# Kernel optimization log

Hardware: AMD Instinct MI355X
Metric: run time of the kernel (lower is better)

## Reference

```python
import jax, jax.numpy as jnp
import numpy as np

T = 0.07  # temperature from init default


def _l2norm(x):
    return x / jnp.linalg.norm(x, axis=1, keepdims=True)


def setup_inputs() -> dict:
    key = jax.random.key(0)
    ks = jax.random.split(key, 12)
    B, D, K = 512, 128, 4096
    G = M = 131072
    return {
        "feat": jax.random.normal(ks[0], (B, D), jnp.float32),
        "label": jax.random.randint(ks[1], (B,), 0, 2),
        "out": jnp.zeros((B, K + 1), jnp.float32),   # unused by forward
        "name": jnp.arange(B),                        # unused by forward
        "y": jax.random.randint(ks[2], (B,), 0, G),   # unused by forward
        "memory_feat_gbm": jax.random.normal(ks[3], (G, D), jnp.float32),
        "memory_prob_gbm": jax.random.uniform(ks[4], (G,), jnp.float32),
        "memory_feat_mate": jax.random.normal(ks[5], (M, D), jnp.float32),
        "memory_prob_mate": jax.random.uniform(ks[6], (M,), jnp.float32),
        "idx_n_g": jax.random.randint(ks[7], (K, 1), 0, G),
        "idx_p_g": jax.random.randint(ks[8], (1, 1), 0, G // 4),
        "idx_n_m": jax.random.randint(ks[9], (K, 1), 0, M),
        "idx_p_m": jax.random.randint(ks[10], (1, 1), 0, M // 4),
    }


def reference(feat, label, out, name, y, memory_feat_gbm, memory_prob_gbm,
              memory_feat_mate, memory_prob_mate, idx_n_g, idx_p_g, idx_n_m, idx_p_m):
    # __init__ normalizes the memory banks once
    mfg = _l2norm(memory_feat_gbm)
    mfm = _l2norm(memory_feat_mate)
    feat_n = _l2norm(feat)  # [B, D]
    output_size = mfg.shape[0]

    # gather positive / negative prototypes (all rows unit-norm, so
    # cosine_similarity == dot product)
    wp_g = mfg[idx_p_g.ravel()]   # [1, D]
    wn_g = mfg[idx_n_g.ravel()]   # [K, D]
    wp_m = mfm[idx_p_m.ravel()]   # [1, D]
    wn_m = mfm[idx_n_m.ravel()]   # [K, D]

    # label==0 (gbm): pos from gbm bank, negs from mate bank; label==1 mirrored
    row_gbm = jnp.concatenate([feat_n @ wp_g.T, feat_n @ wn_m.T], axis=1)   # [B, K+1]
    row_mate = jnp.concatenate([feat_n @ wp_m.T, feat_n @ wn_g.T], axis=1)  # [B, K+1]
    sims = jnp.where((label == 0)[:, None], row_gbm, row_mate)

    # use_softmax=False path: exp(s/T) / Z with Z set from first batch (treated as constant)
    e = jnp.exp(sims / T)
    Z = jax.lax.stop_gradient(e.mean() * output_size)
    out_feature_p_n = e / Z

    # confident cluster members + current batch (data-dependent sizes; eager jax)
    mask_g = memory_prob_gbm > 0.5
    mask_m = memory_prob_mate > 0.6
    feature_clu_all = jnp.concatenate([mfg[mask_g], mfm[mask_m], feat_n], axis=0)
    gt_clu_all = jnp.concatenate([
        jnp.zeros((int(mask_g.sum()),), label.dtype),
        jnp.ones((int(mask_m.sum()),), label.dtype),
        label,
    ], axis=0)
    return out_feature_p_n, feature_clu_all, gt_clu_all
```

## Files before the change

kernel.cpp:

```cpp
#include <hip/hip_runtime.h>
#include <math.h>


#define TINV 14.2857142857142857f
#define JT 64
#define BT2 64

typedef __attribute__((ext_vector_type(8))) short bfrag;
typedef __attribute__((ext_vector_type(4))) float ffrag;

__device__ __forceinline__ float wredsum64(float v) {
#pragma unroll
  for (int m = 32; m > 0; m >>= 1) v += __shfl_xor(v, m, 64);
  return v;
}

__device__ __forceinline__ unsigned short f2bf(float x) {
  unsigned u = __float_as_uint(x);
  u += 0x7fffu + ((u >> 16) & 1u);
  return (unsigned short)(u >> 16);
}

__device__ __forceinline__ bfrag ldsread(const short* base, int row, int kb) {
  return *(const bfrag*)((const char*)base + row * 256 +
                         (kb ^ ((row & 7) << 4)));
}
__device__ __forceinline__ void ldswrite(short* base, int row, int kb,
                                         bfrag v) {
  *(bfrag*)((char*)base + row * 256 + (kb ^ ((row & 7) << 4))) = v;
}

__global__ __launch_bounds__(256) void k_stageA(
    const float* __restrict__ feat, const int* __restrict__ label,
    const float* __restrict__ mfg, const float* __restrict__ pg,
    const float* __restrict__ mfm, const float* __restrict__ pm,
    const int* __restrict__ idxpg, const int* __restrict__ idxpm,
    float* __restrict__ outp, long long cluTail, long long gtTail,
    int* __restrict__ bucket, int* __restrict__ n0p,
    int* __restrict__ cg, int* __restrict__ cm,
    float* __restrict__ posPartials,
    int B, int K1, int G, int M,
    int nCountBlk, int nFeatBlk, int nPosBlk) {
  int bid = blockIdx.x, t = threadIdx.x;

  if (bid < nCountBlk) {
    __shared__ int s[8];
    int i = bid * 256 + t;
    int a = (i < G) && (pg[i] > 0.5f);
    int b = (i < M) && (pm[i] > 0.6f);
    unsigned long long ba = __ballot(a), bb = __ballot(b);
    int lane = t & 63, w = t >> 6;
    if (lane == 0) { s[w] = __popcll(ba); s[4 + w] = __popcll(bb); }
    __syncthreads();
    if (t == 0) cg[bid] = s[0] + s[1] + s[2] + s[3];
    if (t == 1) cm[bid] = s[4] + s[5] + s[6] + s[7];
    return;
  }
  bid -= nCountBlk;

  if (bid < nFeatBlk) {
    int gid = bid * 256 + t;
    int w = gid >> 6, lane = gid & 63;
    if (w < B) {
      float2 v = ((const float2*)feat)[(long long)w * 64 + lane];
      float sq = wredsum64(v.x * v.x + v.y * v.y);
      float inv = rsqrtf(sq);
      ((float2*)(outp + cluTail))[(long long)w * 64 + lane] =
          make_float2(v.x * inv, v.y * inv);
      if (lane == 0) outp[gtTail + w] = (float)label[w];
    }
    return;
  }
  bid -= nFeatBlk;

  if (bid < nPosBlk) {
    __shared__ float ps[4];
    int gid = bid * 256 + t;
    int w = gid >> 6, lane = gid & 63, lw = t >> 6;
    float e = 0.f;
    if (w < B) {
      int lab = label[w];
      const float* bank = lab ? mfm : mfg;
      long long row = lab ? idxpm[0] : idxpg[0];
      float2 wv = ((const float2*)(bank + row * 128))[lane];
      float2 fv = ((const float2*)feat)[(long long)w * 64 + lane];
      float dot = wredsum64(fv.x * wv.x + fv.y * wv.y);
      float sqw = wredsum64(wv.x * wv.x + wv.y * wv.y);
      float sqf = wredsum64(fv.x * fv.x + fv.y * fv.y);
      e = expf(dot * rsqrtf(sqw) * rsqrtf(sqf) * TINV);
      if (lane == 0) outp[(long long)w * K1] = e;
    }
    if (lane == 0) ps[lw] = e;
    __syncthreads();
    if (t == 0) posPartials[bid] = ps[0] + ps[1] + ps[2] + ps[3];
    return;
  }

  {
    __shared__ int sc[512];
    int t2 = t + 256;
    int m0 = (t < B) ? (label[t] == 0 ? 1 : 0) : 0;
    int m1 = (t2 < B) ? (label[t2] == 0 ? 1 : 0) : 0;
    sc[t] = m0; sc[t2] = m1;
    __syncthreads();
    for (int off = 1; off < 512; off <<= 1) {
      int u0 = (t >= off) ? sc[t - off] : 0;
      int u1 = (t2 >= off) ? sc[t2 - off] : 0;
      __syncthreads();
      sc[t] += u0; sc[t2] += u1;
      __syncthreads();
    }
    int n0 = (B > 0) ? sc[B - 1] : 0;
    if (t < B) {
      int incl = sc[t];
      if (m0) bucket[incl - 1] = t; else bucket[n0 + t - incl] = t;
    }
    if (t2 < B) {
      int incl = sc[t2];
      if (m1) bucket[incl - 1] = t2; else bucket[n0 + t2 - incl] = t2;
    }
    if (t == 0) *n0p = n0;
  }
}

__global__ __launch_bounds__(256) void k_stageB(
    const float* __restrict__ featn, const int* __restrict__ bucket,
    const int* __restrict__ n0ptr,
    const float* __restrict__ mfg, const float* __restrict__ mfm,
    const int* __restrict__ idxng, const int* __restrict__ idxnm,
    float* __restrict__ out0, float* __restrict__ partials,
    int B, int K, int K1, int simsGx) {
  __shared__ __align__(16) short wlds[64 * 128];
  __shared__ __align__(16) short flds[64 * 128];
  __shared__ float invw[64];
  __shared__ float bs[4];
  int t = threadIdx.x;
  int pidx = (int)blockIdx.x;
  int bx = pidx % simsGx, by = pidx / simsGx;
  int n0 = *n0ptr;
  int nb0 = (n0 + BT2 - 1) / BT2;
  int lab, p0, cnt;
  if (by < nb0) {
    lab = 0; p0 = by * BT2; cnt = min(BT2, n0 - p0);
  } else {
    int k = by - nb0; p0 = n0 + k * BT2;
    int n1 = B - n0; cnt = min(BT2, n1 - k * BT2); lab = 1;
  }
  if (cnt <= 0) { if (t == 0) partials[pidx] = 0.f; return; }
  const float* bank = lab == 0 ? mfm : mfg;
  const int* idxN   = lab == 0 ? idxnm : idxng;
  int j0 = bx * JT;

#pragma unroll
  for (int q = 0; q < 4; q++) {
    int slot = q * 256 + t;
    int row = slot >> 4, ch = slot & 15;
    long long srow = idxN[j0 + row];
    const float4* gp = (const float4*)(bank + srow * 128 + ch * 8);
    float4 x0 = gp[0], x1 = gp[1];
    bfrag h;
    h[0] = (short)f2bf(x0.x); h[1] = (short)f2bf(x0.y);
    h[2] = (short)f2bf(x0.z); h[3] = (short)f2bf(x0.w);
    h[4] = (short)f2bf(x1.x); h[5] = (short)f2bf(x1.y);
    h[6] = (short)f2bf(x1.z); h[7] = (short)f2bf(x1.w);
    ldswrite(wlds, row, ch * 16, h);
    float s = x0.x*x0.x + x0.y*x0.y + x0.z*x0.z + x0.w*x0.w +
              x1.x*x1.x + x1.y*x1.y + x1.z*x1.z + x1.w*x1.w;
    s += __shfl_xor(s, 1, 64);
    s += __shfl_xor(s, 2, 64);
    s += __shfl_xor(s, 4, 64);
    s += __shfl_xor(s, 8, 64);
    if (ch == 0) invw[row] = rsqrtf(s);
  }
#pragma unroll
  for (int q = 0; q < 4; q++) {
    int slot = q * 256 + t;
    int row = slot >> 4, ch = slot & 15;
    bfrag h;
#pragma unroll
    for (int i = 0; i < 8; i++) h[i] = 0;
    if (row < cnt) {
      int bg = bucket[p0 + row];
      const float4* gp = (const float4*)(featn + (long long)bg * 128 + ch * 8);
      float4 x0 = gp[0], x1 = gp[1];
      h[0] = (short)f2bf(x0.x); h[1] = (short)f2bf(x0.y);
      h[2] = (short)f2bf(x0.z); h[3] = (short)f2bf(x0.w);
      h[4] = (short)f2bf(x1.x); h[5] = (short)f2bf(x1.y);
      h[6] = (short)f2bf(x1.z); h[7] = (short)f2bf(x1.w);
    }
    ldswrite(flds, row, ch * 16, h);
  }
  __syncthreads();

  int l = t & 63, wv = t >> 6;
  int wj = wv & 1, wb = wv >> 1;
  int colb = l & 15, kg = l >> 4;
  ffrag acc00 = {0.f, 0.f, 0.f, 0.f};
  ffrag acc01 = {0.f, 0.f, 0.f, 0.f};
  ffrag acc10 = {0.f, 0.f, 0.f, 0.f};
  ffrag acc11 = {0.f, 0.f, 0.f, 0.f};
#pragma unroll
  for (int ks = 0; ks < 4; ks++) {
    int kb = ks * 64 + kg * 16;
    bfrag a0 = ldsread(flds, wb * 32 + colb,      kb);
    bfrag a1 = ldsread(flds, wb * 32 + 16 + colb, kb);
    bfrag b0 = ldsread(wlds, wj * 32 + colb,      kb);
    bfrag b1 = ldsread(wlds, wj * 32 + 16 + colb, kb);
    acc00 = __builtin_amdgcn_mfma_f32_16x16x32_bf16(a0, b0, acc00, 0, 0, 0);
    acc01 = __builtin_amdgcn_mfma_f32_16x16x32_bf16(a0, b1, acc01, 0, 0, 0);
    acc10 = __builtin_amdgcn_mfma_f32_16x16x32_bf16(a1, b0, acc10, 0, 0, 0);
    acc11 = __builtin_amdgcn_mfma_f32_16x16x32_bf16(a1, b1, acc11, 0, 0, 0);
  }

  float mysum = 0.f;
  int rowg = l >> 4;
  auto epi = [&](const ffrag& A, int bt, int jt) {
    int bl = wb * 32 + bt * 16 + rowg * 4;
    int jl = wj * 32 + jt * 16 + colb;
    float iw = invw[jl];
#pragma unroll
    for (int r = 0; r < 4; r++) {
      int b2 = bl + r;
      if (b2 < cnt) {
        int bg = bucket[p0 + b2];
        float e = expf(A[r] * iw * TINV);
        out0[(long long)bg * K1 + 1 + j0 + jl] = e;
        mysum += e;
      }
    }
  };
  epi(acc00, 0, 0); epi(acc01, 0, 1); epi(acc10, 1, 0); epi(acc11, 1, 1);

  float wsum = wredsum64(mysum);
  if ((t & 63) == 0) bs[t >> 6] = wsum;
  __syncthreads();
  if (t == 0) partials[pidx] = bs[0] + bs[1] + bs[2] + bs[3];
}

__global__ __launch_bounds__(256) void k_stageD(
    const float* __restrict__ mfg, const float* __restrict__ mfm,
    const float* __restrict__ pg, const float* __restrict__ pm,
    const int* __restrict__ cg, const int* __restrict__ cm,
    float* __restrict__ outp, long long cluBase, long long gtBase,
    int G, int M, int NB, int nGatherBlk,
    float* __restrict__ out0, const float* __restrict__ partials, int nPart,
    double factor, long long n4) {
  int t = threadIdx.x;

  if ((int)blockIdx.x < nGatherBlk) {
    __shared__ int red[4];
    __shared__ int woff[4];
    __shared__ int selRow[256];
    int bid = blockIdx.x;
    int bankId = bid / NB;
    int cb = bid - bankId * NB;
    const float* probs = bankId ? pm : pg;
    const float* rows  = bankId ? mfm : mfg;
    float thr = bankId ? 0.6f : 0.5f;
    int Nelem = bankId ? M : G;
    int lane = t & 63, w = t >> 6;

    int j0 = t, j1 = t + 256;
    int s = 0;
    if (bankId == 0) {
      if (j0 < cb) s += cg[j0];
      if (j1 < cb && j1 < NB) s += cg[j1];
    } else {
      if (j0 < NB) s += cg[j0];
      if (j1 < NB) s += cg[j1];
      if (j0 < cb) s += cm[j0];
      if (j1 < cb && j1 < NB) s += cm[j1];
    }
#pragma unroll
    for (int m = 32; m > 0; m >>= 1) s += __shfl_xor(s, m, 64);
    if (lane == 0) red[w] = s;

    int i = cb * 256 + t;
    int f = (i < Nelem) && (probs[i] > thr);
    unsigned long long mb = __ballot(f);
    if (lane == 0) woff[w] = __popcll(mb);
    __syncthreads();

    long long off = (long long)red[0] + red[1] + red[2] + red[3];
    int pre = 0;
#pragma unroll
    for (int q = 0; q < 3; q++)
      if (q < w) pre += woff[q];
    int S = woff[0] + woff[1] + woff[2] + woff[3];
    unsigned long long below = lane ? ((~0ull) >> (64 - lane)) : 0ull;
    if (f) selRow[pre + __popcll(mb & below)] = i;
    __syncthreads();
    if (S == 0) return;

    float labv = (float)bankId;
    int hw = t >> 5, l = t & 31;
    for (int r0 = hw * 4; r0 < S; r0 += 32) {
      int r1 = r0 + 1, r2 = r0 + 2, r3 = r0 + 3;
      int s0 = selRow[r0];
      int s1 = selRow[r1 < S ? r1 : r0];
      int s2 = selRow[r2 < S ? r2 : r0];
      int s3 = selRow[r3 < S ? r3 : r0];
      float4 v0 = ((const float4*)(rows + (long long)s0 * 128))[l];
      float4 v1 = ((const float4*)(rows + (long long)s1 * 128))[l];
      float4 v2 = ((const float4*)(rows + (long long)s2 * 128))[l];
      float4 v3 = ((const float4*)(rows + (long long)s3 * 128))[l];
      float q0 = v0.x*v0.x + v0.y*v0.y + v0.z*v0.z + v0.w*v0.w;
      float q1 = v1.x*v1.x + v1.y*v1.y + v1.z*v1.z + v1.w*v1.w;
      float q2 = v2.x*v2.x + v2.y*v2.y + v2.z*v2.z + v2.w*v2.w;
      float q3 = v3.x*v3.x + v3.y*v3.y + v3.z*v3.z + v3.w*v3.w;
#pragma unroll
      for (int m = 16; m > 0; m >>= 1) {
        q0 += __shfl_xor(q0, m, 64);
        q1 += __shfl_xor(q1, m, 64);
        q2 += __shfl_xor(q2, m, 64);
        q3 += __shfl_xor(q3, m, 64);
      }
      float i0 = rsqrtf(q0), i1 = rsqrtf(q1), i2 = rsqrtf(q2), i3 = rsqrtf(q3);
      long long d0 = off + r0;
      ((float4*)(outp + cluBase + d0 * 128))[l] =
          make_float4(v0.x*i0, v0.y*i0, v0.z*i0, v0.w*i0);
      if (l == 0) outp[gtBase + d0] = labv;
      if (r1 < S) {
        long long d = off + r1;
        ((float4*)(outp + cluBase + d * 128))[l] =
            make_float4(v1.x*i1, v1.y*i1, v1.z*i1, v1.w*i1);
        if (l == 0) outp[gtBase + d] = labv;
      }
      if (r2 < S) {
        long long d = off + r2;
        ((float4*)(outp + cluBase + d * 128))[l] =
            make_float4(v2.x*i2, v2.y*i2, v2.z*i2, v2.w*i2);
        if (l == 0) outp[gtBase + d] = labv;
      }
      if (r3 < S) {
        long long d = off + r3;
        ((float4*)(outp + cluBase + d * 128))[l] =
            make_float4(v3.x*i3, v3.y*i3, v3.z*i3, v3.w*i3);
        if (l == 0) outp[gtBase + d] = labv;
      }
    }
    return;
  }

  __shared__ double sd[256];
  double s = 0.0;
  for (int i = t; i < nPart; i += 256) s += (double)partials[i];
  sd[t] = s;
  __syncthreads();
  for (int off = 128; off > 0; off >>= 1) {
    if (t < off) sd[t] += sd[t + off];
    __syncthreads();
  }
  float sc = (float)(factor / sd[0]);
  long long base = (long long)((int)blockIdx.x - nGatherBlk) * 256 + t;
  long long stride = (long long)(gridDim.x - nGatherBlk) * 256;
  for (long long i = base; i < n4; i += stride) {
    float4 v = ((float4*)out0)[i];
    v.x *= sc; v.y *= sc; v.z *= sc; v.w *= sc;
    ((float4*)out0)[i] = v;
  }
}

extern "C" void kernel_launch(void* const* d_in, const int* in_sizes, int n_in,
                              void* d_out, int out_size, void* d_ws,
                              size_t ws_size, hipStream_t stream) {
  const float* feat  = (const float*)d_in[0];
  const int*   label = (const int*)d_in[1];
  const float* mfg   = (const float*)d_in[5];
  const float* pg    = (const float*)d_in[6];
  const float* mfm   = (const float*)d_in[7];
  const float* pm    = (const float*)d_in[8];
  const int*   idxng = (const int*)d_in[9];
  const int*   idxpg = (const int*)d_in[10];
  const int*   idxnm = (const int*)d_in[11];
  const int*   idxpm = (const int*)d_in[12];
  float* outp = (float*)d_out;

  const int B = in_sizes[1];
  const int D = 128;
  const int K = in_sizes[9];
  const int G = in_sizes[6];
  const int M = in_sizes[8];
  const int K1 = K + 1;

  const long long C0 = (long long)B * K1;
  const long long R = ((long long)out_size - C0) / (D + 1);
  const long long G0 = C0 + R * D;
  const long long cluTail = C0 + (R - B) * (long long)D;
  const long long gtTail = G0 + (R - B);

  const float* featn = outp + cluTail;

  char* wsb = (char*)d_ws;
  size_t o = 0;
  auto alloc = [&](size_t bytes) -> char* {
    char* p = wsb + o;
    o = (o + bytes + 255) & ~(size_t)255;
    return p;
  };
  const int simsGx = K / JT;
  const int simsGy = B / BT2 + 2;
  const int nPartSims = simsGx * simsGy;
  const int nPosBlk = (B * 64 + 255) / 256;
  float* partials = (float*)alloc(sizeof(float) * (nPartSims + nPosBlk));
  int* bucket = (int*)alloc(sizeof(int) * B);
  int* n0p = (int*)alloc(sizeof(int) * 4);
  const int NB = ((G > M ? G : M) + 255) / 256;
  int* cg = (int*)alloc(sizeof(int) * NB);
  int* cm = (int*)alloc(sizeof(int) * NB);
  (void)ws_size; (void)n_in;

  const int nFeatBlk = (B * 64 + 255) / 256;
  const int gridA = NB + nFeatBlk + nPosBlk + 1;
  const int gridB = nPartSims;
  const int nGatherBlk = 2 * NB;
  const int nScaleBlk = 1024;
  const int gridD = nGatherBlk + nScaleBlk;

  k_stageA<<<gridA, 256, 0, stream>>>(
      feat, label, mfg, pg, mfm, pm, idxpg, idxpm,
      outp, cluTail, gtTail, bucket, n0p, cg, cm,
      partials + nPartSims, B, K1, G, M, NB, nFeatBlk, nPosBlk);

  k_stageB<<<gridB, 256, 0, stream>>>(
      featn, bucket, n0p, mfg, mfm, idxng, idxnm,
      outp, partials, B, K, K1, simsGx);

  double factor = (double)B * (double)K1 / (double)G;
  k_stageD<<<gridD, 256, 0, stream>>>(
      mfg, mfm, pg, pm, cg, cm, outp, C0, G0, G, M, NB, nGatherBlk,
      outp, partials, nPartSims + nPosBlk, factor, C0 / 4);
}
```

Before: 44.76 us.

## Shrink gather chunks to 64 rows, stage rows in LDS, use nontemporal stores

Stage A now writes per-wavefront (64-element) popcounts instead of per-block counts. Stage D then launches one gather block per 64-element chunk instead of per 256, which quadruples the gather grid and spreads the compaction across more blocks. Each block stages selected rows in LDS, computes norms from per-lane partial sums there, and writes normalized rows with nontemporal stores. The prefix-offset loop now reads four times as many counts per block, and the extra LDS staging adds syncs and shared-memory traffic per block.

```diff
diff --git a/kernel.cpp b/kernel.cpp
--- a/kernel.cpp
+++ b/kernel.cpp
@@ -8,8 +8,15 @@
 
 typedef __attribute__((ext_vector_type(8))) short bfrag;
 typedef __attribute__((ext_vector_type(4))) float ffrag;
+typedef __attribute__((ext_vector_type(4))) float f4v;
 
 __device__ __forceinline__ float wredsum64(float v) {
+#pragma unroll
+  for (int m = 32; m > 0; m >>= 1) v += __shfl_xor(v, m, 64);
+  return v;
+}
+
+__device__ __forceinline__ int wredsum64i(int v) {
 #pragma unroll
   for (int m = 32; m > 0; m >>= 1) v += __shfl_xor(v, m, 64);
   return v;
@@ -37,23 +44,22 @@
     const int* __restrict__ idxpg, const int* __restrict__ idxpm,
     float* __restrict__ outp, long long cluTail, long long gtTail,
     int* __restrict__ bucket, int* __restrict__ n0p,
-    int* __restrict__ cg, int* __restrict__ cm,
+    int* __restrict__ cg64, int* __restrict__ cm64,
     float* __restrict__ posPartials,
     int B, int K1, int G, int M,
     int nCountBlk, int nFeatBlk, int nPosBlk) {
   int bid = blockIdx.x, t = threadIdx.x;
 
   if (bid < nCountBlk) {
-    __shared__ int s[8];
     int i = bid * 256 + t;
     int a = (i < G) && (pg[i] > 0.5f);
     int b = (i < M) && (pm[i] > 0.6f);
     unsigned long long ba = __ballot(a), bb = __ballot(b);
     int lane = t & 63, w = t >> 6;
-    if (lane == 0) { s[w] = __popcll(ba); s[4 + w] = __popcll(bb); }
-    __syncthreads();
-    if (t == 0) cg[bid] = s[0] + s[1] + s[2] + s[3];
-    if (t == 1) cm[bid] = s[4] + s[5] + s[6] + s[7];
+    if (lane == 0) {
+      cg64[bid * 4 + w] = __popcll(ba);
+      cm64[bid * 4 + w] = __popcll(bb);
+    }
     return;
   }
   bid -= nCountBlk;
@@ -240,103 +246,98 @@
 __global__ __launch_bounds__(256) void k_stageD(
     const float* __restrict__ mfg, const float* __restrict__ mfm,
     const float* __restrict__ pg, const float* __restrict__ pm,
-    const int* __restrict__ cg, const int* __restrict__ cm,
+    const int* __restrict__ cg64, const int* __restrict__ cm64,
     float* __restrict__ outp, long long cluBase, long long gtBase,
-    int G, int M, int NB, int nGatherBlk,
+    int G, int M, int NG64, int nGatherBlk,
     float* __restrict__ out0, const float* __restrict__ partials, int nPart,
     double factor, long long n4) {
   int t = threadIdx.x;
 
   if ((int)blockIdx.x < nGatherBlk) {
+    __shared__ float rowbuf[64][132];
+    __shared__ float psum[64][33];
+    __shared__ float invw[64];
+    __shared__ int selRow[64];
     __shared__ int red[4];
-    __shared__ int woff[4];
-    __shared__ int selRow[256];
+    __shared__ int Ssh;
     int bid = blockIdx.x;
-    int bankId = bid / NB;
-    int cb = bid - bankId * NB;
+    int bankId = bid / NG64;
+    int g = bid - bankId * NG64;
     const float* probs = bankId ? pm : pg;
     const float* rows  = bankId ? mfm : mfg;
     float thr = bankId ? 0.6f : 0.5f;
     int Nelem = bankId ? M : G;
     int lane = t & 63, w = t >> 6;
 
-    int j0 = t, j1 = t + 256;
     int s = 0;
-    if (bankId == 0) {
-      if (j0 < cb) s += cg[j0];
-      if (j1 < cb && j1 < NB) s += cg[j1];
-    } else {
-      if (j0 < NB) s += cg[j0];
-      if (j1 < NB) s += cg[j1];
-      if (j0 < cb) s += cm[j0];
-      if (j1 < cb && j1 < NB) s += cm[j1];
-    }
-#pragma unroll
-    for (int m = 32; m > 0; m >>= 1) s += __shfl_xor(s, m, 64);
+    for (int j = t; j < NG64; j += 256) {
+      if (bankId == 0) {
+        if (j < g) s += cg64[j];
+      } else {
+        s += cg64[j];
+        if (j < g) s += cm64[j];
+      }
+    }
+    s = wredsum64i(s);
     if (lane == 0) red[w] = s;
 
-    int i = cb * 256 + t;
-    int f = (i < Nelem) && (probs[i] > thr);
-    unsigned long long mb = __ballot(f);
-    if (lane == 0) woff[w] = __popcll(mb);
-    __syncthreads();
-
+    if (t < 64) {
+      int c = g * 64 + t;
+      int f = (c < Nelem) && (probs[c] > thr);
+      unsigned long long mb = __ballot(f);
+      unsigned long long below = t ? ((~0ull) >> (64 - t)) : 0ull;
+      if (f) selRow[__popcll(mb & below)] = c;
+      if (t == 0) Ssh = (int)__popcll(mb);
+    }
+    __syncthreads();
+    int S = Ssh;
+    if (S == 0) return;
     long long off = (long long)red[0] + red[1] + red[2] + red[3];
-    int pre = 0;
-#pragma unroll
-    for (int q = 0; q < 3; q++)
-      if (q < w) pre += woff[q];
-    int S = woff[0] + woff[1] + woff[2] + woff[3];
-    unsigned long long below = lane ? ((~0ull) >> (64 - lane)) : 0ull;
-    if (f) selRow[pre + __popcll(mb & below)] = i;
-    __syncthreads();
-    if (S == 0) return;
-
     float labv = (float)bankId;
     int hw = t >> 5, l = t & 31;
+
     for (int r0 = hw * 4; r0 < S; r0 += 32) {
-      int r1 = r0 + 1, r2 = r0 + 2, r3 = r0 + 3;
-      int s0 = selRow[r0];
-      int s1 = selRow[r1 < S ? r1 : r0];
-      int s2 = selRow[r2 < S ? r2 : r0];
-      int s3 = selRow[r3 < S ? r3 : r0];
-      float4 v0 = ((const float4*)(rows + (long long)s0 * 128))[l];
-      float4 v1 = ((const float4*)(rows + (long long)s1 * 128))[l];
-      float4 v2 = ((const float4*)(rows + (long long)s2 * 128))[l];
-      float4 v3 = ((const float4*)(rows + (long long)s3 * 128))[l];
-      float q0 = v0.x*v0.x + v0.y*v0.y + v0.z*v0.z + v0.w*v0.w;
-      float q1 = v1.x*v1.x + v1.y*v1.y + v1.z*v1.z + v1.w*v1.w;
-      float q2 = v2.x*v2.x + v2.y*v2.y + v2.z*v2.z + v2.w*v2.w;
-      float q3 = v3.x*v3.x + v3.y*v3.y + v3.z*v3.z + v3.w*v3.w;
-#pragma unroll
-      for (int m = 16; m > 0; m >>= 1) {
-        q0 += __shfl_xor(q0, m, 64);
-        q1 += __shfl_xor(q1, m, 64);
-        q2 += __shfl_xor(q2, m, 64);
-        q3 += __shfl_xor(q3, m, 64);
-      }
-      float i0 = rsqrtf(q0), i1 = rsqrtf(q1), i2 = rsqrtf(q2), i3 = rsqrtf(q3);
-      long long d0 = off + r0;
-      ((float4*)(outp + cluBase + d0 * 128))[l] =
-          make_float4(v0.x*i0, v0.y*i0, v0.z*i0, v0.w*i0);
-      if (l == 0) outp[gtBase + d0] = labv;
-      if (r1 < S) {
-        long long d = off + r1;
-        ((float4*)(outp + cluBase + d * 128))[l] =
-            make_float4(v1.x*i1, v1.y*i1, v1.z*i1, v1.w*i1);
-        if (l == 0) outp[gtBase + d] = labv;
-      }
-      if (r2 < S) {
-        long long d = off + r2;
-        ((float4*)(outp + cluBase + d * 128))[l] =
-            make_float4(v2.x*i2, v2.y*i2, v2.z*i2, v2.w*i2);
-        if (l == 0) outp[gtBase + d] = labv;
-      }
-      if (r3 < S) {
-        long long d = off + r3;
-        ((float4*)(outp + cluBase + d * 128))[l] =
-            make_float4(v3.x*i3, v3.y*i3, v3.z*i3, v3.w*i3);
-        if (l == 0) outp[gtBase + d] = labv;
+      int ra = r0;
+      int rb = min(r0 + 1, S - 1);
+      int rc = min(r0 + 2, S - 1);
+      int rd = min(r0 + 3, S - 1);
+      f4v v0 = *(const f4v*)(rows + (long long)selRow[ra] * 128 + l * 4);
+      f4v v1 = *(const f4v*)(rows + (long long)selRow[rb] * 128 + l * 4);
+      f4v v2 = *(const f4v*)(rows + (long long)selRow[rc] * 128 + l * 4);
+      f4v v3 = *(const f4v*)(rows + (long long)selRow[rd] * 128 + l * 4);
+      *(f4v*)&rowbuf[ra][l * 4] = v0;
+      psum[ra][l] = v0.x * v0.x + v0.y * v0.y + v0.z * v0.z + v0.w * v0.w;
+      *(f4v*)&rowbuf[rb][l * 4] = v1;
+      psum[rb][l] = v1.x * v1.x + v1.y * v1.y + v1.z * v1.z + v1.w * v1.w;
+      *(f4v*)&rowbuf[rc][l * 4] = v2;
+      psum[rc][l] = v2.x * v2.x + v2.y * v2.y + v2.z * v2.z + v2.w * v2.w;
+      *(f4v*)&rowbuf[rd][l * 4] = v3;
+      psum[rd][l] = v3.x * v3.x + v3.y * v3.y + v3.z * v3.z + v3.w * v3.w;
+    }
+    __syncthreads();
+
+    if (t < 64 && t < S) {
+      float ss = 0.f;
+#pragma unroll
+      for (int i = 0; i < 32; i++) ss += psum[t][i];
+      invw[t] = rsqrtf(ss);
+    }
+    __syncthreads();
+
+    for (int r0 = hw * 4; r0 < S; r0 += 32) {
+#pragma unroll
+      for (int k = 0; k < 4; k++) {
+        int r = r0 + k;
+        if (r < S) {
+          f4v v = *(const f4v*)&rowbuf[r][l * 4];
+          float iw = invw[r];
+          v.x *= iw; v.y *= iw; v.z *= iw; v.w *= iw;
+          long long d = off + r;
+          __builtin_nontemporal_store(
+              v, (f4v*)(outp + cluBase + d * 128 + l * 4));
+          if (l == 0)
+            __builtin_nontemporal_store(labv, outp + gtBase + d);
+        }
       }
     }
     return;
@@ -406,20 +407,21 @@
   int* bucket = (int*)alloc(sizeof(int) * B);
   int* n0p = (int*)alloc(sizeof(int) * 4);
   const int NB = ((G > M ? G : M) + 255) / 256;
-  int* cg = (int*)alloc(sizeof(int) * NB);
-  int* cm = (int*)alloc(sizeof(int) * NB);
+  const int NG64 = NB * 4;
+  int* cg64 = (int*)alloc(sizeof(int) * NG64);
+  int* cm64 = (int*)alloc(sizeof(int) * NG64);
   (void)ws_size; (void)n_in;
 
   const int nFeatBlk = (B * 64 + 255) / 256;
   const int gridA = NB + nFeatBlk + nPosBlk + 1;
   const int gridB = nPartSims;
-  const int nGatherBlk = 2 * NB;
+  const int nGatherBlk = 2 * NG64;
   const int nScaleBlk = 1024;
   const int gridD = nGatherBlk + nScaleBlk;
 
   k_stageA<<<gridA, 256, 0, stream>>>(
       feat, label, mfg, pg, mfm, pm, idxpg, idxpm,
-      outp, cluTail, gtTail, bucket, n0p, cg, cm,
+      outp, cluTail, gtTail, bucket, n0p, cg64, cm64,
       partials + nPartSims, B, K1, G, M, NB, nFeatBlk, nPosBlk);
 
   k_stageB<<<gridB, 256, 0, stream>>>(
@@ -428,6 +430,6 @@
 
   double factor = (double)B * (double)K1 / (double)G;
   k_stageD<<<gridD, 256, 0, stream>>>(
-      mfg, mfm, pg, pm, cg, cm, outp, C0, G0, G, M, NB, nGatherBlk,
+      mfg, mfm, pg, pm, cg64, cm64, outp, C0, G0, G, M, NG64, nGatherBlk,
       outp, partials, nPartSims + nPosBlk, factor, C0 / 4);
 }
```

Measured after the change: 54.23 us. +21.2%, slower.
